# Kernel tuning notes

Hardware: AMD Instinct MI355X
Metric: run time of the kernel (lower is better)

Reference implementation:

```python
import jax, jax.numpy as jnp
import numpy as np

N_NODES = 100000
N_EDGES = 3200000
N_FEATS = 512
HIDDEN = 16
N_CLASSES = 40


def gcn_conv(x, edge_index, W, b):
    """PyG-style GCNConv: linear -> symmetric-normalized scatter-add -> bias."""
    n = x.shape[0]
    src, dst = edge_index[0], edge_index[1]
    # add self-loops
    loop = jnp.arange(n, dtype=src.dtype)
    src = jnp.concatenate([src, loop])
    dst = jnp.concatenate([dst, loop])
    # symmetric normalization deg^{-1/2}[src] * deg^{-1/2}[dst]
    deg = jax.ops.segment_sum(jnp.ones_like(src, dtype=x.dtype), dst, num_segments=n)
    dinv = jnp.where(deg > 0, jax.lax.rsqrt(jnp.maximum(deg, 1.0)), 0.0)
    norm = dinv[src] * dinv[dst]  # [E+N]
    h = x @ W                     # [N, out]
    msg = h[src] * norm[:, None]  # gather + scale, [E+N, out]
    out = jax.ops.segment_sum(msg, dst, num_segments=n)  # scatter-add at targets
    return out + b


def setup_inputs() -> dict:
    key = jax.random.key(0)
    k1, k2, k3, k4 = jax.random.split(key, 4)
    x = jax.random.normal(k1, (N_NODES, N_FEATS), dtype=jnp.float32)
    edge_index = jax.random.randint(k2, (2, N_EDGES), 0, N_NODES, dtype=jnp.int64)
    # Glorot-ish scaled weights
    W1 = jax.random.normal(k3, (N_FEATS, HIDDEN), dtype=jnp.float32) * (1.0 / np.sqrt(N_FEATS))
    b1 = jnp.zeros((HIDDEN,), dtype=jnp.float32)
    W2 = jax.random.normal(k4, (HIDDEN, N_CLASSES), dtype=jnp.float32) * (1.0 / np.sqrt(HIDDEN))
    b2 = jnp.zeros((N_CLASSES,), dtype=jnp.float32)
    return {"x": x, "edge_index": edge_index, "W1": W1, "b1": b1, "W2": W2, "b2": b2}


def reference(x, edge_index, W1, b1, W2, b2):
    h = gcn_conv(x, edge_index, W1, b1)
    h = jax.nn.relu(h)
    # dropout is identity in eval mode
    h = gcn_conv(h, edge_index, W2, b2)
    return jax.nn.log_softmax(h, axis=1)
```

## Files before the change

kernel.cpp:

```cpp
#include <hip/hip_runtime.h>
#include <hip/hip_bf16.h>

#define NN 100000
#define NE 3200000
#define NF 512
#define NH 16
#define NC 40
#define BKT_SH 8
#define NBKT 391
#define CAP 8960
#define HISTB 1536
#define CHUNK_H 2084
#define SCATB 256
#define ROWS_PER_SCAT 6
#define CHUNK_S 12504
#define GEMMB 1563

typedef __attribute__((ext_vector_type(4))) float f32x4;
typedef __attribute__((ext_vector_type(8))) short bf16x8;

static __device__ __forceinline__ unsigned short f2b(float f) {
    unsigned int u = __float_as_uint(f);
    u += 0x7FFFu + ((u >> 16) & 1u);
    return (unsigned short)(u >> 16);
}
static __device__ __forceinline__ float b2f(unsigned short u) {
    return __uint_as_float(((unsigned int)u) << 16);
}


__global__ void __launch_bounds__(256) kA_gemm_hist(const float* __restrict__ x,
                                                    const float* __restrict__ W1,
                                                    const int* __restrict__ ei,
                                                    unsigned short* __restrict__ h1,
                                                    int* __restrict__ histG) {
    __shared__ int smem[4096];
    int tid = threadIdx.x;
    if (blockIdx.x < HISTB) {
        int* h = smem;
        for (int i = tid; i < NBKT; i += 256) h[i] = 0;
        __syncthreads();
        int r = blockIdx.x;
        int e0 = r * CHUNK_H, e1 = min(NE, e0 + CHUNK_H);
        for (int e = e0 + tid; e < e1; e += 256)
            atomicAdd(&h[((unsigned)ei[NE + e]) >> BKT_SH], 1);
        __syncthreads();
        for (int i = tid; i < NBKT; i += 256)
            histG[r * NBKT + i] = h[i];
        __syncthreads();
    }
    unsigned short* wl = (unsigned short*)smem;
    for (int idx = tid; idx < 8192; idx += 256) {
        int s = idx >> 9;
        int l = (idx >> 3) & 63;
        int e = idx & 7;
        int k = s * 32 + (l >> 4) * 8 + e;
        wl[idx] = f2b(W1[k * 16 + (l & 15)]);
    }
    __syncthreads();
    int wave = tid >> 6;
    int l = tid & 63;
    int m0 = blockIdx.x * 64 + wave * 16;
    if (m0 >= NN) return;
    int row = m0 + (l & 15);
    int krow = (l >> 4) * 8;
    const float* xr = x + (size_t)row * NF + krow;
    const unsigned short* wf = wl + l * 8;
    f32x4 acc = {0.f, 0.f, 0.f, 0.f};
#pragma unroll 4
    for (int s = 0; s < 16; ++s) {
        f32x4 xa = *(const f32x4*)(xr + s * 32);
        f32x4 xb = *(const f32x4*)(xr + s * 32 + 4);
        union { bf16x8 v; unsigned short u[8]; } a;
        a.u[0] = f2b(xa.x); a.u[1] = f2b(xa.y); a.u[2] = f2b(xa.z); a.u[3] = f2b(xa.w);
        a.u[4] = f2b(xb.x); a.u[5] = f2b(xb.y); a.u[6] = f2b(xb.z); a.u[7] = f2b(xb.w);
        bf16x8 b = *(const bf16x8*)(wf + s * 512);
        acc = __builtin_amdgcn_mfma_f32_16x16x32_bf16(a.v, b, acc, 0, 0, 0);
    }
#pragma unroll
    for (int r = 0; r < 4; ++r) {
        int orow = m0 + (l >> 4) * 4 + r;
        h1[(size_t)orow * NH + (l & 15)] = f2b(acc[r]);
    }
}


__global__ void __launch_bounds__(512) k_colscan(const int* __restrict__ histG,
                                                 int* __restrict__ ofsG,
                                                 int* __restrict__ bcnt) {
    __shared__ int sh[512];
    int k = blockIdx.x;
    int t = threadIdx.x;
    int base = t * 3;
    int a0 = histG[(size_t)(base + 0) * NBKT + k];
    int a1 = histG[(size_t)(base + 1) * NBKT + k];
    int a2 = histG[(size_t)(base + 2) * NBKT + k];
    int s = a0 + a1 + a2;
    sh[t] = s;
    __syncthreads();
    for (int off = 1; off < 512; off <<= 1) {
        int add = (t >= off) ? sh[t - off] : 0;
        __syncthreads();
        sh[t] += add;
        __syncthreads();
    }
    int excl = sh[t] - s;
    if ((t & 1) == 0) ofsG[(size_t)k * SCATB + (t >> 1)] = excl;
    if (t == 511) bcnt[k] = sh[t];
}


__global__ void k_bscan(const int* __restrict__ bcnt, int* __restrict__ bptr,
                        int* __restrict__ rowptr) {
    __shared__ int sh[512];
    int t = threadIdx.x;
    int v = (t < NBKT) ? bcnt[t] : 0;
    sh[t] = v;
    __syncthreads();
    for (int off = 1; off < 512; off <<= 1) {
        int add = (t >= off) ? sh[t - off] : 0;
        __syncthreads();
        sh[t] += add;
        __syncthreads();
    }
    if (t < NBKT) bptr[t] = sh[t] - v;
    if (t == 0) { bptr[NBKT] = NE; rowptr[NN] = NE; }
}


__global__ void __launch_bounds__(1024) k_msscatter(const int* __restrict__ ei,
                                                    const int* __restrict__ bptr,
                                                    const int* __restrict__ ofsG,
                                                    unsigned int* __restrict__ pairs) {
    __shared__ int lcur[NBKT];
    int b = blockIdx.x;
    for (int k = threadIdx.x; k < NBKT; k += 1024)
        lcur[k] = bptr[k] + ofsG[(size_t)k * SCATB + b];
    __syncthreads();
    int e0 = b * CHUNK_S, e1 = min(NE, e0 + CHUNK_S);
    for (int e = e0 + threadIdx.x; e < e1; e += 1024) {
        unsigned int s = (unsigned int)ei[e];
        unsigned int d = (unsigned int)ei[NE + e];
        int pos = atomicAdd(&lcur[d >> BKT_SH], 1);
        pairs[pos] = s | ((d & 255u) << 17);
    }
}


__global__ void __launch_bounds__(1024) k_bsort(const unsigned int* __restrict__ pairs,
                                                const int* __restrict__ bptr,
                                                int* __restrict__ rowptr,
                                                float* __restrict__ dinv,
                                                int* __restrict__ ssrc) {
    __shared__ unsigned int ein[CAP];
    __shared__ unsigned int srt[CAP];
    __shared__ int lcnt[256], lofs[256], lcur[256];
    int b = blockIdx.x;
    int t = threadIdx.x;
    int s0 = bptr[b], s1 = bptr[b + 1];
    int n = s1 - s0;
    for (int i = t; i < n; i += 1024) ein[i] = pairs[s0 + i];
    if (t < 256) lcnt[t] = 0;
    __syncthreads();
    for (int i = t; i < n; i += 1024) atomicAdd(&lcnt[ein[i] >> 17], 1);
    __syncthreads();
    if (t < 256) lofs[t] = lcnt[t];
    __syncthreads();
    for (int off = 1; off < 256; off <<= 1) {
        int add = 0;
        if (t < 256 && t >= off) add = lofs[t - off];
        __syncthreads();
        if (t < 256) lofs[t] += add;
        __syncthreads();
    }
    if (t < 256) {
        int excl = lofs[t] - lcnt[t];
        lcur[t] = excl;
        int node = b * 256 + t;
        if (node < NN) {
            rowptr[node] = s0 + excl;
            dinv[node] = rsqrtf((float)(lcnt[t] + 1));
        }
    }
    __syncthreads();
    for (int i = t; i < n; i += 1024) {
        unsigned int v = ein[i];
        int pos = atomicAdd(&lcur[v >> 17], 1);
        srt[pos] = v & 0x1FFFFu;
    }
    __syncthreads();
    for (int i = t; i < n; i += 1024) ssrc[s0 + i] = (int)srt[i];
}


__global__ void __launch_bounds__(256) k_agg1(const unsigned short* __restrict__ hs,
                                              const int* __restrict__ rowptr,
                                              const int* __restrict__ ssrc,
                                              const float* __restrict__ dinv,
                                              const float* __restrict__ b1,
                                              unsigned short* __restrict__ r1) {
    int l = threadIdx.x & 63;
    int node = blockIdx.x * 4 + (threadIdx.x >> 6);
    int j = l & 15;
    int ec = l >> 4;
    float di = dinv[node];
    int s = rowptr[node];
    int e1 = rowptr[node + 1];
    float acc = (ec == 0) ? b2f(hs[(size_t)node * NH + j]) * di : 0.0f;
#pragma unroll 4
    for (int e = s + ec; e < e1; e += 4) {
        int src = ssrc[e];
        acc += b2f(hs[(size_t)src * NH + j]) * dinv[src];
    }
    acc += __shfl_xor(acc, 16, 64);
    acc += __shfl_xor(acc, 32, 64);
    if (ec == 0) {
        float o = fmaxf(acc * di + b1[j], 0.0f) * di;
        r1[(size_t)node * NH + j] = f2b(o);
    }
}


__global__ void __launch_bounds__(256) k_agg2(const unsigned short* __restrict__ rs,
                                              const int* __restrict__ rowptr,
                                              const int* __restrict__ ssrc,
                                              const float* __restrict__ dinv,
                                              const float* __restrict__ W2,
                                              const float* __restrict__ b2,
                                              float* __restrict__ out) {
    __shared__ float w[NH * NC];
    __shared__ float bb[NC];
    int t = threadIdx.x;
    for (int i = t; i < NH * NC; i += 256) w[i] = W2[i];
    if (t < NC) bb[t] = b2[t];
    __syncthreads();
    int l = t & 63;
    int node = blockIdx.x * 4 + (t >> 6);
    int j = l & 15;
    int ec = l >> 4;
    float di = dinv[node];
    int s = rowptr[node];
    int e1 = rowptr[node + 1];
    float acc = (ec == 0) ? b2f(rs[(size_t)node * NH + j]) : 0.0f;
#pragma unroll 4
    for (int e = s + ec; e < e1; e += 4) {
        int src = ssrc[e];
        acc += b2f(rs[(size_t)src * NH + j]);
    }
    acc += __shfl_xor(acc, 16, 64);
    acc += __shfl_xor(acc, 32, 64);
    float zv = acc * di;
    float lg = (l < NC) ? bb[l] : -1e30f;
#pragma unroll
    for (int k = 0; k < NH; ++k) {
        float zk = __shfl(zv, k, 64);
        if (l < NC) lg += zk * w[k * NC + l];
    }
    float mx = lg;
#pragma unroll
    for (int off = 1; off < 64; off <<= 1) mx = fmaxf(mx, __shfl_xor(mx, off, 64));
    float ex = (l < NC) ? __expf(lg - mx) : 0.0f;
    float sm = ex;
#pragma unroll
    for (int off = 1; off < 64; off <<= 1) sm += __shfl_xor(sm, off, 64);
    if (l < NC) out[(size_t)node * NC + l] = lg - mx - __logf(sm);
}


extern "C" void kernel_launch(void* const* d_in, const int* in_sizes, int n_in,
                              void* d_out, int out_size, void* d_ws, size_t ws_size,
                              hipStream_t stream) {
    const float* x  = (const float*)d_in[0];
    const int*   ei = (const int*)d_in[1];
    const float* W1 = (const float*)d_in[2];
    const float* b1 = (const float*)d_in[3];
    const float* W2 = (const float*)d_in[4];
    const float* b2 = (const float*)d_in[5];
    float* out = (float*)d_out;

    char* ws = (char*)d_ws;
    size_t off = 0;
    auto alloc = [&](size_t bytes) -> void* {
        void* p = ws + off;
        off += (bytes + 255) & ~(size_t)255;
        return p;
    };
    int* histG      = (int*)alloc((size_t)HISTB * NBKT * 4);
    int* ofsG       = (int*)alloc((size_t)NBKT * SCATB * 4);
    int* bcnt       = (int*)alloc((size_t)NBKT * 4);
    int* bptr       = (int*)alloc((size_t)(NBKT + 1) * 4);
    int* rowptr     = (int*)alloc((size_t)(NN + 1) * 4);
    float* dinv     = (float*)alloc((size_t)NN * 4);
    unsigned int* pairs = (unsigned int*)alloc((size_t)NE * 4);
    int* ssrc       = (int*)alloc((size_t)NE * 4);
    unsigned short* h1  = (unsigned short*)alloc((size_t)NN * NH * 2);
    unsigned short* r1  = (unsigned short*)alloc((size_t)NN * NH * 2);

    kA_gemm_hist<<<GEMMB, 256, 0, stream>>>(x, W1, ei, h1, histG);
    k_colscan<<<NBKT, 512, 0, stream>>>(histG, ofsG, bcnt);
    k_bscan<<<1, 512, 0, stream>>>(bcnt, bptr, rowptr);
    k_msscatter<<<SCATB, 1024, 0, stream>>>(ei, bptr, ofsG, pairs);
    k_bsort<<<NBKT, 1024, 0, stream>>>(pairs, bptr, rowptr, dinv, ssrc);
    k_agg1<<<NN / 4, 256, 0, stream>>>(h1, rowptr, ssrc, dinv, b1, r1);
    k_agg2<<<NN / 4, 256, 0, stream>>>(r1, rowptr, ssrc, dinv, W2, b2, out);
}
```

Baseline: 222.5 us.

## Vectorize aggregation gathers to 8-byte loads and fold bucket scan into colscan

The aggregation kernels now have each lane load four bf16 features at once, so one wave covers 16 edges per iteration instead of 4, with a wider shuffle reduction at the end. This cuts the number of load instructions and the loop trips spent on irregular gathers. The separate single-block bucket scan kernel is removed: the last colscan block, found with an atomic counter that the first kernel resets, now does the scan. That saves one launch but adds a threadfence and an atomic to every colscan block.

```diff
diff --git a/kernel.cpp b/kernel.cpp
--- a/kernel.cpp
+++ b/kernel.cpp
@@ -12,12 +12,12 @@
 #define HISTB 1536
 #define CHUNK_H 2084
 #define SCATB 256
-#define ROWS_PER_SCAT 6
 #define CHUNK_S 12504
 #define GEMMB 1563
 
 typedef __attribute__((ext_vector_type(4))) float f32x4;
 typedef __attribute__((ext_vector_type(8))) short bf16x8;
+typedef __attribute__((ext_vector_type(4))) unsigned short u16x4;
 
 static __device__ __forceinline__ unsigned short f2b(float f) {
     unsigned int u = __float_as_uint(f);
@@ -33,9 +33,11 @@
                                                     const float* __restrict__ W1,
                                                     const int* __restrict__ ei,
                                                     unsigned short* __restrict__ h1,
-                                                    int* __restrict__ histG) {
+                                                    int* __restrict__ histG,
+                                                    int* __restrict__ done) {
     __shared__ int smem[4096];
     int tid = threadIdx.x;
+    if (blockIdx.x == 0 && tid == 0) *done = 0;
     if (blockIdx.x < HISTB) {
         int* h = smem;
         for (int i = tid; i < NBKT; i += 256) h[i] = 0;
@@ -87,8 +89,12 @@
 
 __global__ void __launch_bounds__(512) k_colscan(const int* __restrict__ histG,
                                                  int* __restrict__ ofsG,
-                                                 int* __restrict__ bcnt) {
+                                                 int* __restrict__ bcnt,
+                                                 int* __restrict__ bptr,
+                                                 int* __restrict__ rowptr,
+                                                 int* __restrict__ done) {
     __shared__ int sh[512];
+    __shared__ int isLast;
     int k = blockIdx.x;
     int t = threadIdx.x;
     int base = t * 3;
@@ -107,14 +113,13 @@
     int excl = sh[t] - s;
     if ((t & 1) == 0) ofsG[(size_t)k * SCATB + (t >> 1)] = excl;
     if (t == 511) bcnt[k] = sh[t];
-}
-
-
-__global__ void k_bscan(const int* __restrict__ bcnt, int* __restrict__ bptr,
-                        int* __restrict__ rowptr) {
-    __shared__ int sh[512];
-    int t = threadIdx.x;
+    __threadfence();
+    __syncthreads();
+    if (t == 0) isLast = (atomicAdd(done, 1) == NBKT - 1);
+    __syncthreads();
+    if (!isLast) return;
     int v = (t < NBKT) ? bcnt[t] : 0;
+    __syncthreads();
     sh[t] = v;
     __syncthreads();
     for (int off = 1; off < 512; off <<= 1) {
@@ -201,22 +206,39 @@
                                               unsigned short* __restrict__ r1) {
     int l = threadIdx.x & 63;
     int node = blockIdx.x * 4 + (threadIdx.x >> 6);
-    int j = l & 15;
-    int ec = l >> 4;
+    int q = l & 3;
+    int slice = l >> 2;
     float di = dinv[node];
     int s = rowptr[node];
     int e1 = rowptr[node + 1];
-    float acc = (ec == 0) ? b2f(hs[(size_t)node * NH + j]) * di : 0.0f;
-#pragma unroll 4
-    for (int e = s + ec; e < e1; e += 4) {
+    f32x4 acc = {0.f, 0.f, 0.f, 0.f};
+    if (slice == 0) {
+        u16x4 v = *(const u16x4*)(hs + ((size_t)node << 4) + (q << 2));
+        acc[0] = b2f(v.x) * di; acc[1] = b2f(v.y) * di;
+        acc[2] = b2f(v.z) * di; acc[3] = b2f(v.w) * di;
+    }
+    for (int e = s + slice; e < e1; e += 16) {
         int src = ssrc[e];
-        acc += b2f(hs[(size_t)src * NH + j]) * dinv[src];
-    }
-    acc += __shfl_xor(acc, 16, 64);
-    acc += __shfl_xor(acc, 32, 64);
-    if (ec == 0) {
-        float o = fmaxf(acc * di + b1[j], 0.0f) * di;
-        r1[(size_t)node * NH + j] = f2b(o);
+        float ds = dinv[src];
+        u16x4 v = *(const u16x4*)(hs + ((size_t)src << 4) + (q << 2));
+        acc[0] += b2f(v.x) * ds; acc[1] += b2f(v.y) * ds;
+        acc[2] += b2f(v.z) * ds; acc[3] += b2f(v.w) * ds;
+    }
+#pragma unroll
+    for (int off = 4; off < 64; off <<= 1) {
+        acc[0] += __shfl_xor(acc[0], off, 64);
+        acc[1] += __shfl_xor(acc[1], off, 64);
+        acc[2] += __shfl_xor(acc[2], off, 64);
+        acc[3] += __shfl_xor(acc[3], off, 64);
+    }
+    if (l < 4) {
+        f32x4 bq = *(const f32x4*)(b1 + (q << 2));
+        u16x4 o;
+        o.x = f2b(fmaxf(acc[0] * di + bq.x, 0.0f) * di);
+        o.y = f2b(fmaxf(acc[1] * di + bq.y, 0.0f) * di);
+        o.z = f2b(fmaxf(acc[2] * di + bq.z, 0.0f) * di);
+        o.w = f2b(fmaxf(acc[3] * di + bq.w, 0.0f) * di);
+        *(u16x4*)(r1 + ((size_t)node << 4) + (q << 2)) = o;
     }
 }
 
@@ -236,24 +258,33 @@
     __syncthreads();
     int l = t & 63;
     int node = blockIdx.x * 4 + (t >> 6);
-    int j = l & 15;
-    int ec = l >> 4;
+    int q = l & 3;
+    int slice = l >> 2;
     float di = dinv[node];
     int s = rowptr[node];
     int e1 = rowptr[node + 1];
-    float acc = (ec == 0) ? b2f(rs[(size_t)node * NH + j]) : 0.0f;
-#pragma unroll 4
-    for (int e = s + ec; e < e1; e += 4) {
+    f32x4 acc = {0.f, 0.f, 0.f, 0.f};
+    if (slice == 0) {
+        u16x4 v = *(const u16x4*)(rs + ((size_t)node << 4) + (q << 2));
+        acc[0] = b2f(v.x); acc[1] = b2f(v.y); acc[2] = b2f(v.z); acc[3] = b2f(v.w);
+    }
+    for (int e = s + slice; e < e1; e += 16) {
         int src = ssrc[e];
-        acc += b2f(rs[(size_t)src * NH + j]);
-    }
-    acc += __shfl_xor(acc, 16, 64);
-    acc += __shfl_xor(acc, 32, 64);
-    float zv = acc * di;
+        u16x4 v = *(const u16x4*)(rs + ((size_t)src << 4) + (q << 2));
+        acc[0] += b2f(v.x); acc[1] += b2f(v.y); acc[2] += b2f(v.z); acc[3] += b2f(v.w);
+    }
+#pragma unroll
+    for (int off = 4; off < 64; off <<= 1) {
+        acc[0] += __shfl_xor(acc[0], off, 64);
+        acc[1] += __shfl_xor(acc[1], off, 64);
+        acc[2] += __shfl_xor(acc[2], off, 64);
+        acc[3] += __shfl_xor(acc[3], off, 64);
+    }
+    acc[0] *= di; acc[1] *= di; acc[2] *= di; acc[3] *= di;
     float lg = (l < NC) ? bb[l] : -1e30f;
 #pragma unroll
     for (int k = 0; k < NH; ++k) {
-        float zk = __shfl(zv, k, 64);
+        float zk = __shfl(acc[k & 3], k >> 2, 64);
         if (l < NC) lg += zk * w[k * NC + l];
     }
     float mx = lg;
@@ -291,14 +322,14 @@
     int* bptr       = (int*)alloc((size_t)(NBKT + 1) * 4);
     int* rowptr     = (int*)alloc((size_t)(NN + 1) * 4);
     float* dinv     = (float*)alloc((size_t)NN * 4);
+    int* done       = (int*)alloc(256);
     unsigned int* pairs = (unsigned int*)alloc((size_t)NE * 4);
     int* ssrc       = (int*)alloc((size_t)NE * 4);
     unsigned short* h1  = (unsigned short*)alloc((size_t)NN * NH * 2);
     unsigned short* r1  = (unsigned short*)alloc((size_t)NN * NH * 2);
 
-    kA_gemm_hist<<<GEMMB, 256, 0, stream>>>(x, W1, ei, h1, histG);
-    k_colscan<<<NBKT, 512, 0, stream>>>(histG, ofsG, bcnt);
-    k_bscan<<<1, 512, 0, stream>>>(bcnt, bptr, rowptr);
+    kA_gemm_hist<<<GEMMB, 256, 0, stream>>>(x, W1, ei, h1, histG, done);
+    k_colscan<<<NBKT, 512, 0, stream>>>(histG, ofsG, bcnt, bptr, rowptr, done);
     k_msscatter<<<SCATB, 1024, 0, stream>>>(ei, bptr, ofsG, pairs);
     k_bsort<<<NBKT, 1024, 0, stream>>>(pairs, bptr, rowptr, dinv, ssrc);
     k_agg1<<<NN / 4, 256, 0, stream>>>(h1, rowptr, ssrc, dinv, b1, r1);
```

Measured after the change: 264.3 us. +18.8%, slower.

## Fuse bucket scan into colscan via last-block atomic and prefetch GEMM x rows

Applied to the files above, without the earlier changes.

Removes the separate single-block k_bscan launch. The last k_colscan block to finish, detected with a threadfence plus an atomic counter that kA_gemm_hist resets, now performs the bucket prefix scan. The GEMM loop is also restructured to load all 16 x slices up front in two register-buffered halves, so memory loads overlap the MFMA work. This saves one kernel launch and exposes more load-level parallelism, at the cost of higher register pressure and a serialized tail in one colscan block.

```diff
diff --git a/kernel.cpp b/kernel.cpp
--- a/kernel.cpp
+++ b/kernel.cpp
@@ -12,7 +12,6 @@
 #define HISTB 1536
 #define CHUNK_H 2084
 #define SCATB 256
-#define ROWS_PER_SCAT 6
 #define CHUNK_S 12504
 #define GEMMB 1563
 
@@ -33,9 +32,11 @@
                                                     const float* __restrict__ W1,
                                                     const int* __restrict__ ei,
                                                     unsigned short* __restrict__ h1,
-                                                    int* __restrict__ histG) {
+                                                    int* __restrict__ histG,
+                                                    int* __restrict__ done) {
     __shared__ int smem[4096];
     int tid = threadIdx.x;
+    if (blockIdx.x == 0 && tid == 0) *done = 0;
     if (blockIdx.x < HISTB) {
         int* h = smem;
         for (int i = tid; i < NBKT; i += 256) h[i] = 0;
@@ -66,15 +67,31 @@
     int krow = (l >> 4) * 8;
     const float* xr = x + (size_t)row * NF + krow;
     const unsigned short* wf = wl + l * 8;
+
+    f32x4 xa[8], xb[8];
+#pragma unroll
+    for (int s = 0; s < 8; ++s) {
+        xa[s] = *(const f32x4*)(xr + s * 32);
+        xb[s] = *(const f32x4*)(xr + s * 32 + 4);
+    }
     f32x4 acc = {0.f, 0.f, 0.f, 0.f};
-#pragma unroll 4
-    for (int s = 0; s < 16; ++s) {
-        f32x4 xa = *(const f32x4*)(xr + s * 32);
-        f32x4 xb = *(const f32x4*)(xr + s * 32 + 4);
+#pragma unroll
+    for (int s = 0; s < 8; ++s) {
+        f32x4 na = *(const f32x4*)(xr + (s + 8) * 32);
+        f32x4 nb = *(const f32x4*)(xr + (s + 8) * 32 + 4);
         union { bf16x8 v; unsigned short u[8]; } a;
-        a.u[0] = f2b(xa.x); a.u[1] = f2b(xa.y); a.u[2] = f2b(xa.z); a.u[3] = f2b(xa.w);
-        a.u[4] = f2b(xb.x); a.u[5] = f2b(xb.y); a.u[6] = f2b(xb.z); a.u[7] = f2b(xb.w);
+        a.u[0] = f2b(xa[s].x); a.u[1] = f2b(xa[s].y); a.u[2] = f2b(xa[s].z); a.u[3] = f2b(xa[s].w);
+        a.u[4] = f2b(xb[s].x); a.u[5] = f2b(xb[s].y); a.u[6] = f2b(xb[s].z); a.u[7] = f2b(xb[s].w);
         bf16x8 b = *(const bf16x8*)(wf + s * 512);
+        acc = __builtin_amdgcn_mfma_f32_16x16x32_bf16(a.v, b, acc, 0, 0, 0);
+        xa[s] = na; xb[s] = nb;
+    }
+#pragma unroll
+    for (int s = 0; s < 8; ++s) {
+        union { bf16x8 v; unsigned short u[8]; } a;
+        a.u[0] = f2b(xa[s].x); a.u[1] = f2b(xa[s].y); a.u[2] = f2b(xa[s].z); a.u[3] = f2b(xa[s].w);
+        a.u[4] = f2b(xb[s].x); a.u[5] = f2b(xb[s].y); a.u[6] = f2b(xb[s].z); a.u[7] = f2b(xb[s].w);
+        bf16x8 b = *(const bf16x8*)(wf + (s + 8) * 512);
         acc = __builtin_amdgcn_mfma_f32_16x16x32_bf16(a.v, b, acc, 0, 0, 0);
     }
 #pragma unroll
@@ -87,8 +104,12 @@
 
 __global__ void __launch_bounds__(512) k_colscan(const int* __restrict__ histG,
                                                  int* __restrict__ ofsG,
-                                                 int* __restrict__ bcnt) {
+                                                 int* __restrict__ bcnt,
+                                                 int* __restrict__ bptr,
+                                                 int* __restrict__ rowptr,
+                                                 int* __restrict__ done) {
     __shared__ int sh[512];
+    __shared__ int isLast;
     int k = blockIdx.x;
     int t = threadIdx.x;
     int base = t * 3;
@@ -107,14 +128,13 @@
     int excl = sh[t] - s;
     if ((t & 1) == 0) ofsG[(size_t)k * SCATB + (t >> 1)] = excl;
     if (t == 511) bcnt[k] = sh[t];
-}
-
-
-__global__ void k_bscan(const int* __restrict__ bcnt, int* __restrict__ bptr,
-                        int* __restrict__ rowptr) {
-    __shared__ int sh[512];
-    int t = threadIdx.x;
+    __threadfence();
+    __syncthreads();
+    if (t == 0) isLast = (atomicAdd(done, 1) == NBKT - 1);
+    __syncthreads();
+    if (!isLast) return;
     int v = (t < NBKT) ? bcnt[t] : 0;
+    __syncthreads();
     sh[t] = v;
     __syncthreads();
     for (int off = 1; off < 512; off <<= 1) {
@@ -291,14 +311,14 @@
     int* bptr       = (int*)alloc((size_t)(NBKT + 1) * 4);
     int* rowptr     = (int*)alloc((size_t)(NN + 1) * 4);
     float* dinv     = (float*)alloc((size_t)NN * 4);
+    int* done       = (int*)alloc(256);
     unsigned int* pairs = (unsigned int*)alloc((size_t)NE * 4);
     int* ssrc       = (int*)alloc((size_t)NE * 4);
     unsigned short* h1  = (unsigned short*)alloc((size_t)NN * NH * 2);
     unsigned short* r1  = (unsigned short*)alloc((size_t)NN * NH * 2);
 
-    kA_gemm_hist<<<GEMMB, 256, 0, stream>>>(x, W1, ei, h1, histG);
-    k_colscan<<<NBKT, 512, 0, stream>>>(histG, ofsG, bcnt);
-    k_bscan<<<1, 512, 0, stream>>>(bcnt, bptr, rowptr);
+    kA_gemm_hist<<<GEMMB, 256, 0, stream>>>(x, W1, ei, h1, histG, done);
+    k_colscan<<<NBKT, 512, 0, stream>>>(histG, ofsG, bcnt, bptr, rowptr, done);
     k_msscatter<<<SCATB, 1024, 0, stream>>>(ei, bptr, ofsG, pairs);
     k_bsort<<<NBKT, 1024, 0, stream>>>(pairs, bptr, rowptr, dinv, ssrc);
     k_agg1<<<NN / 4, 256, 0, stream>>>(h1, rowptr, ssrc, dinv, b1, r1);
```

After: 267.5 us. 20.3% more time.

## Stage x tiles into LDS with async global_load_lds double buffering in GEMM

Applied to the files above, without the earlier changes.

The first-layer GEMM now copies 64-column chunks of x into a double-buffered, XOR-swizzled LDS tile using direct global-to-LDS loads. It then feeds the MFMA from LDS instead of loading row fragments straight from global memory. The goal is to overlap the next chunk's load with compute and get coalesced full-row reads. In exchange it uses 48KB of shared memory, which may reduce occupancy, and adds a barrier per chunk.

```diff
diff --git a/kernel.cpp b/kernel.cpp
--- a/kernel.cpp
+++ b/kernel.cpp
@@ -12,9 +12,10 @@
 #define HISTB 1536
 #define CHUNK_H 2084
 #define SCATB 256
-#define ROWS_PER_SCAT 6
 #define CHUNK_S 12504
 #define GEMMB 1563
+#define KC 64
+#define NCHUNK 8
 
 typedef __attribute__((ext_vector_type(4))) float f32x4;
 typedef __attribute__((ext_vector_type(8))) short bf16x8;
@@ -34,10 +35,10 @@
                                                     const int* __restrict__ ei,
                                                     unsigned short* __restrict__ h1,
                                                     int* __restrict__ histG) {
-    __shared__ int smem[4096];
+    __shared__ char smem[49152];
     int tid = threadIdx.x;
     if (blockIdx.x < HISTB) {
-        int* h = smem;
+        int* h = (int*)smem;
         for (int i = tid; i < NBKT; i += 256) h[i] = 0;
         __syncthreads();
         int r = blockIdx.x;
@@ -57,30 +58,60 @@
         int k = s * 32 + (l >> 4) * 8 + e;
         wl[idx] = f2b(W1[k * 16 + (l & 15)]);
     }
-    __syncthreads();
-    int wave = tid >> 6;
+    float* xbuf = (float*)(smem + 16384);
+    int w = tid >> 6;
     int l = tid & 63;
-    int m0 = blockIdx.x * 64 + wave * 16;
-    if (m0 >= NN) return;
-    int row = m0 + (l & 15);
-    int krow = (l >> 4) * 8;
-    const float* xr = x + (size_t)row * NF + krow;
-    const unsigned short* wf = wl + l * 8;
+    int m0row = blockIdx.x * 64;
+    int srow = tid >> 4;
+    int sunit = tid & 15;
+
+    auto stage = [&](int buf, int c) {
+        float* dst = xbuf + buf * 4096;
+        int kb = c * KC;
+#pragma unroll
+        for (int t = 0; t < 4; ++t) {
+            int row = t * 16 + srow;
+            int grow = m0row + row;
+            if (grow >= NN) grow = NN - 1;
+            int colbyte = (sunit * 16) ^ ((row & 7) << 5);
+            const float* g = x + (size_t)grow * NF + kb + (colbyte >> 2);
+            float* ldsb = dst + t * 1024 + w * 256;
+            __builtin_amdgcn_global_load_lds(
+                (const __attribute__((address_space(1))) void*)g,
+                (__attribute__((address_space(3))) void*)ldsb, 16, 0, 0);
+        }
+    };
+
+    int rowl = w * 16 + (l & 15);
+    int hq = l >> 4;
+    int rbase = rowl * 64;
     f32x4 acc = {0.f, 0.f, 0.f, 0.f};
-#pragma unroll 4
-    for (int s = 0; s < 16; ++s) {
-        f32x4 xa = *(const f32x4*)(xr + s * 32);
-        f32x4 xb = *(const f32x4*)(xr + s * 32 + 4);
-        union { bf16x8 v; unsigned short u[8]; } a;
-        a.u[0] = f2b(xa.x); a.u[1] = f2b(xa.y); a.u[2] = f2b(xa.z); a.u[3] = f2b(xa.w);
-        a.u[4] = f2b(xb.x); a.u[5] = f2b(xb.y); a.u[6] = f2b(xb.z); a.u[7] = f2b(xb.w);
-        bf16x8 b = *(const bf16x8*)(wf + s * 512);
-        acc = __builtin_amdgcn_mfma_f32_16x16x32_bf16(a.v, b, acc, 0, 0, 0);
-    }
-#pragma unroll
-    for (int r = 0; r < 4; ++r) {
-        int orow = m0 + (l >> 4) * 4 + r;
-        h1[(size_t)orow * NH + (l & 15)] = f2b(acc[r]);
+
+    stage(0, 0);
+    __syncthreads();
+    for (int c = 0; c < NCHUNK; ++c) {
+        if (c + 1 < NCHUNK) stage((c + 1) & 1, c + 1);
+        const float* src = xbuf + (c & 1) * 4096;
+#pragma unroll
+        for (int sl = 0; sl < 2; ++sl) {
+            int colbyte = (sl * 128 + hq * 32) ^ ((rowl & 7) << 5);
+            const float* p = src + rbase + (colbyte >> 2);
+            f32x4 xa = *(const f32x4*)p;
+            f32x4 xb = *(const f32x4*)(p + 4);
+            union { bf16x8 v; unsigned short u[8]; } a;
+            a.u[0] = f2b(xa.x); a.u[1] = f2b(xa.y); a.u[2] = f2b(xa.z); a.u[3] = f2b(xa.w);
+            a.u[4] = f2b(xb.x); a.u[5] = f2b(xb.y); a.u[6] = f2b(xb.z); a.u[7] = f2b(xb.w);
+            bf16x8 b = *(const bf16x8*)(wl + l * 8 + (c * 2 + sl) * 512);
+            acc = __builtin_amdgcn_mfma_f32_16x16x32_bf16(a.v, b, acc, 0, 0, 0);
+        }
+        __syncthreads();
+    }
+    if (m0row + w * 16 < NN) {
+#pragma unroll
+        for (int r = 0; r < 4; ++r) {
+            int orow = m0row + w * 16 + hq * 4 + r;
+            h1[(size_t)orow * NH + (l & 15)] = f2b(acc[r]);
+        }
     }
 }
 
```

New measurement: 224.6 us. Within noise of the previous version (+1.0%).
